# Optimization experiments

Hardware: AMD Instinct MI355X
Metric: run time of the kernel (lower is better)

Reference implementation:

```python
import jax, jax.numpy as jnp
import numpy as np

EMBED_DIM = 4
SEQ_LEN = 14 * 14


def setup_inputs() -> dict:
    key = jax.random.key(0)
    ks = jax.random.split(key, 7)
    B = 32768
    x = jax.random.normal(ks[0], (B, 1, 28, 28), dtype=jnp.float32)
    conv_w = jax.random.normal(ks[1], (4, 1, 2, 2), dtype=jnp.float32) * 0.5
    conv_b = jax.random.normal(ks[2], (4,), dtype=jnp.float32) * 0.1
    rotation_params = jax.random.uniform(ks[3], (16,), dtype=jnp.float32)
    entangle_params = jax.random.uniform(ks[4], (16,), dtype=jnp.float32)
    lin_w = jax.random.normal(ks[5], (10, 784), dtype=jnp.float32) * 0.05
    lin_b = jax.random.normal(ks[6], (10,), dtype=jnp.float32) * 0.05
    return {"x": x, "conv_w": conv_w, "conv_b": conv_b,
            "rotation_params": rotation_params, "entangle_params": entangle_params,
            "lin_w": lin_w, "lin_b": lin_b}


def reference(x, conv_w, conv_b, rotation_params, entangle_params, lin_w, lin_b):
    B = x.shape[0]
    # Quanvolution filter: Conv2d(1,4,k=2,s=2) -> [B,4,14,14]
    feat = jax.lax.conv_general_dilated(
        x, conv_w, window_strides=(2, 2), padding='VALID',
        dimension_numbers=('NCHW', 'OIHW', 'NCHW'))
    feat = feat + conv_b[None, :, None, None]
    # flatten (channel-major like torch .view) then reshape to [B, 196, 4]
    feat = feat.reshape(B, -1).reshape(B, SEQ_LEN, EMBED_DIM)
    # mean embedding per sample: [B, 4]
    mean_embeds = feat.mean(axis=1)
    # classical self-attention on a length-1 sequence per sample
    R = rotation_params.reshape(EMBED_DIM, EMBED_DIM)
    E = entangle_params.reshape(EMBED_DIM, EMBED_DIM)
    q = mean_embeds @ R                               # [B, 4]
    k = mean_embeds @ E                               # [B, 4]
    scores = jnp.einsum('bd,bd->b', q, k) / jnp.sqrt(jnp.float32(EMBED_DIM))
    # softmax over a single-element axis (seq_len == 1) -> all ones, kept for fidelity
    scores = jax.nn.softmax(scores[:, None], axis=-1)  # [B, 1]
    attn_weights = scores * mean_embeds                # [B, 4] (== mean_embeds)
    # broadcast-scale features and classify
    feat = (feat * attn_weights[:, None, :]).reshape(B, -1)  # [B, 784]
    logits = feat @ lin_w.T + lin_b
    return jax.nn.log_softmax(logits, axis=-1)
```

## Files before the change

### kernel.cpp

```cpp
#include <hip/hip_runtime.h>


typedef __attribute__((ext_vector_type(8))) short bf16x8;
typedef __attribute__((ext_vector_type(4))) float f32x4;
typedef __attribute__((ext_vector_type(4))) unsigned int uint4v;

union BU { uint4v u; bf16x8 b; };

__device__ __forceinline__ unsigned short f2bf(float f) {
  unsigned u = __float_as_uint(f);
  unsigned r = u + 0x7FFFu + ((u >> 16) & 1u);
  return (unsigned short)(r >> 16);
}
__device__ __forceinline__ float bf2f(unsigned short h) {
  return __uint_as_float((unsigned)h << 16);
}

#define CST_F 38400
#define A_F   38440

__global__ void qsac_prep(const float* __restrict__ cw, const float* __restrict__ cb,
                          const float* __restrict__ lw, float* __restrict__ wsf) {
  unsigned short* gt = (unsigned short*)wsf;
  const int i = blockIdx.x * 256 + threadIdx.x;
  const int e = i & 7, ln = (i >> 3) & 63, c = i >> 9;
  const int t = c / 3, nt = c - t * 3;
  const int col = nt * 16 + (ln & 15);
  const int k = t * 32 + (ln >> 4) * 8 + e;
  float val = 0.f;
  if (k < 784) {
    const int r = k / 28, cc = k - r * 28;
    const int kh = r & 1, kw = cc & 1;
    const int p = (r >> 1) * 14 + (cc >> 1);
    const int dpix = (2 * ((r >> 1) & 1) + (cc >> 1)) & 3;
    const int cd = col / 12, cj = col - cd * 12;
    if (cd == dpix) {
      const float w0 = cw[(kh << 1) + kw],     w1 = cw[4 + (kh << 1) + kw],
                  w2 = cw[8 + (kh << 1) + kw], w3 = cw[12 + (kh << 1) + kw];
      if (cj < 10)
        val = w0 * lw[cj * 784 + p]       + w1 * lw[cj * 784 + 196 + p] +
              w2 * lw[cj * 784 + 392 + p] + w3 * lw[cj * 784 + 588 + p];
      else if (cj == 10)
        val = (w0 + w1 + w2 + w3) * (1.0f / 196.0f);
    }
  }
  const unsigned short hh = f2bf(val);
  gt[c * 1024 + ln * 8 + e] = hh;
  gt[c * 1024 + 512 + ln * 8 + e] = f2bf(val - bf2f(hh));

  if (blockIdx.x == 0) {
    const int u = threadIdx.x;
    if (u < 40) {
      const int d = u / 10, j = u - (u / 10) * 10;
      const float b0 = cb[0], b1 = cb[1], b2 = cb[2], b3 = cb[3];
      float s = 0.f;
#pragma unroll 7
      for (int q = d; q < 196; q += 4)
        s += b0 * lw[j * 784 + q]       + b1 * lw[j * 784 + 196 + q] +
             b2 * lw[j * 784 + 392 + q] + b3 * lw[j * 784 + 588 + q];
      wsf[CST_F + u] = s;
    } else if (u == 40) {
      wsf[A_F] = (cb[0] + cb[1] + cb[2] + cb[3]) * 0.25f;
    }
  }
}

__global__ __launch_bounds__(1024)
__attribute__((amdgpu_waves_per_eu(4, 4))) void qsac_main(
    const float* __restrict__ x, const float* __restrict__ wsf,
    const float* __restrict__ lin_b, float* __restrict__ out) {
  __shared__ unsigned int smemu[38400];

  const int tid = threadIdx.x;
  const int lane = tid & 63;
  const int wid = __builtin_amdgcn_readfirstlane(tid >> 6);
  const int strip = wid & 7;
  const int khalf = wid >> 3;
  const int nn = lane & 15, kb = lane >> 4;
  const int sbase = blockIdx.x * 128 + strip * 16;
  const float* xrow = x + (size_t)(sbase + nn) * 784;

  {
    const char* wsb = (const char*)wsf;
#pragma unroll
    for (int i = 0; i < 9; ++i) {
      const int cbase = i * 1024 + wid * 64;
      __builtin_amdgcn_global_load_lds(
          (const __attribute__((address_space(1))) unsigned int*)
              (wsb + (size_t)(cbase + lane) * 16),
          (__attribute__((address_space(3))) unsigned int*)&smemu[cbase * 4],
          16, 0, 0);
    }
    if (wid < 6) {
      const int cbase = 9216 + wid * 64;
      __builtin_amdgcn_global_load_lds(
          (const __attribute__((address_space(1))) unsigned int*)
              (wsb + (size_t)(cbase + lane) * 16),
          (__attribute__((address_space(3))) unsigned int*)&smemu[cbase * 4],
          16, 0, 0);
    }
  }
  __syncthreads();

  f32x4 acc[3];
#pragma unroll
  for (int nt = 0; nt < 3; ++nt) acc[nt] = (f32x4){0.f, 0.f, 0.f, 0.f};

  auto tile = [&](const float4& a, const float4& b2, int t) {
    BU bh[3], bl[3];
    const unsigned int* bb = smemu + t * 1536 + lane * 4;
#pragma unroll
    for (int nt = 0; nt < 3; ++nt) {
      bh[nt].u = *(const uint4v*)(bb + nt * 512);
      bl[nt].u = *(const uint4v*)(bb + nt * 512 + 256);
    }
    const float v[8] = {a.x, a.y, a.z, a.w, b2.x, b2.y, b2.z, b2.w};
    bf16x8 Ah, Al;
#pragma unroll
    for (int e = 0; e < 8; ++e) {
      const unsigned short hh = f2bf(v[e]);
      Ah[e] = (short)hh;
      Al[e] = (short)f2bf(v[e] - bf2f(hh));
    }
#pragma unroll
    for (int nt = 0; nt < 3; ++nt) {
      acc[nt] = __builtin_amdgcn_mfma_f32_16x16x32_bf16(Ah, bh[nt].b, acc[nt], 0, 0, 0);
      acc[nt] = __builtin_amdgcn_mfma_f32_16x16x32_bf16(Al, bh[nt].b, acc[nt], 0, 0, 0);
      acc[nt] = __builtin_amdgcn_mfma_f32_16x16x32_bf16(Ah, bl[nt].b, acc[nt], 0, 0, 0);
    }
  };

  auto ldA = [&](int t, float4& a, float4& b2) {
    const int ka = t * 32 + kb * 8;
    const int kc = (ka < 784) ? ka : 0;
    a = *(const float4*)(xrow + kc);
    b2 = *(const float4*)(xrow + kc + 4);
  };

  const int t0 = khalf ? 12 : 0;
  const int t1 = khalf ? 25 : 12;
  float4 xa, xb, na, nb;
  ldA(t0, xa, xb);
#pragma unroll 1
  for (int t = t0; t < t1 - 1; ++t) {
    ldA(t + 1, na, nb);
    tile(xa, xb, t);
    xa = na; xb = nb;
  }
  tile(xa, xb, t1 - 1);

  __syncthreads();
  float* red = (float*)smemu;
  if (khalf == 1) {
#pragma unroll
    for (int nt = 0; nt < 3; ++nt)
#pragma unroll
      for (int rg = 0; rg < 4; ++rg)
        red[(strip * 64 + lane) * 12 + nt * 4 + rg] = acc[nt][rg];
  }
  __syncthreads();
  if (khalf == 0) {
#pragma unroll
    for (int nt = 0; nt < 3; ++nt)
#pragma unroll
      for (int rg = 0; rg < 4; ++rg)
        acc[nt][rg] += red[(strip * 64 + lane) * 12 + nt * 4 + rg];

    float* cx = (float*)smemu + 8192 + strip * (16 * 52);
#pragma unroll
    for (int nt = 0; nt < 3; ++nt)
#pragma unroll
      for (int rg = 0; rg < 4; ++rg)
        cx[(kb * 4 + rg) * 52 + nt * 16 + nn] = acc[nt][rg];
    __builtin_amdgcn_wave_barrier();

    if (lane < 16) {
      float Y[48];
#pragma unroll
      for (int q = 0; q < 12; ++q) {
        const float4 t4 = *(const float4*)&cx[lane * 52 + q * 4];
        Y[q * 4 + 0] = t4.x; Y[q * 4 + 1] = t4.y;
        Y[q * 4 + 2] = t4.z; Y[q * 4 + 3] = t4.w;
      }
      const float a = wsf[A_F];
      float M[4];
#pragma unroll
      for (int d = 0; d < 4; ++d) M[d] = a + Y[d * 12 + 10];
      float logits[10];
#pragma unroll
      for (int j = 0; j < 10; ++j) {
        float vv = lin_b[j];
#pragma unroll
        for (int d = 0; d < 4; ++d)
          vv += M[d] * (wsf[CST_F + d * 10 + j] + Y[d * 12 + j]);
        logits[j] = vv;
      }
      float mx = logits[0];
#pragma unroll
      for (int j = 1; j < 10; ++j) mx = fmaxf(mx, logits[j]);
      float se = 0.f;
#pragma unroll
      for (int j = 0; j < 10; ++j) se += __expf(logits[j] - mx);
      const float lse = mx + __logf(se);
      float* op = out + (size_t)(sbase + lane) * 10;
#pragma unroll
      for (int j = 0; j < 10; ++j) op[j] = logits[j] - lse;
    }
  }
}

extern "C" void kernel_launch(void* const* d_in, const int* in_sizes, int n_in,
                              void* d_out, int out_size, void* d_ws, size_t ws_size,
                              hipStream_t stream) {
  (void)n_in; (void)ws_size; (void)out_size;
  const float* x = (const float*)d_in[0];
  const float* conv_w = (const float*)d_in[1];
  const float* conv_b = (const float*)d_in[2];
  const float* lin_w = (const float*)d_in[5];
  const float* lin_b = (const float*)d_in[6];
  float* out = (float*)d_out;
  float* wsf = (float*)d_ws;

  hipLaunchKernelGGL(qsac_prep, dim3(150), dim3(256), 0, stream,
                     conv_w, conv_b, lin_w, wsf);

  const int B = in_sizes[0] / 784;
  const int nblk = B / 128;
  hipLaunchKernelGGL(qsac_main, dim3(nblk), dim3(1024), 0, stream,
                     x, wsf, lin_b, out);
}
```

Before: 30.35 us.

## Drop split-bf16 error compensation and halve block size to 512 threads

```diff
diff --git a/kernel.cpp b/kernel.cpp
--- a/kernel.cpp
+++ b/kernel.cpp
@@ -6,18 +6,15 @@
 typedef __attribute__((ext_vector_type(4))) unsigned int uint4v;
 
 union BU { uint4v u; bf16x8 b; };
-
-__device__ __forceinline__ unsigned short f2bf(float f) {
-  unsigned u = __float_as_uint(f);
-  unsigned r = u + 0x7FFFu + ((u >> 16) & 1u);
-  return (unsigned short)(r >> 16);
-}
-__device__ __forceinline__ float bf2f(unsigned short h) {
-  return __uint_as_float((unsigned)h << 16);
-}
-
-#define CST_F 38400
-#define A_F   38440
+union AB { unsigned int u[4]; bf16x8 b; };
+
+__device__ __forceinline__ unsigned rne16(float f) {
+  const unsigned u = __float_as_uint(f);
+  return (u + 0x7FFFu + ((u >> 16) & 1u)) >> 16;
+}
+
+#define CST_F 19200
+#define A_F   19240
 
 __global__ void qsac_prep(const float* __restrict__ cw, const float* __restrict__ cb,
                           const float* __restrict__ lw, float* __restrict__ wsf) {
@@ -44,9 +41,7 @@
         val = (w0 + w1 + w2 + w3) * (1.0f / 196.0f);
     }
   }
-  const unsigned short hh = f2bf(val);
-  gt[c * 1024 + ln * 8 + e] = hh;
-  gt[c * 1024 + 512 + ln * 8 + e] = f2bf(val - bf2f(hh));
+  gt[c * 512 + ln * 8 + e] = (unsigned short)rne16(val);
 
   if (blockIdx.x == 0) {
     const int u = threadIdx.x;
@@ -65,39 +60,33 @@
   }
 }
 
-__global__ __launch_bounds__(1024)
+__global__ __launch_bounds__(512)
 __attribute__((amdgpu_waves_per_eu(4, 4))) void qsac_main(
     const float* __restrict__ x, const float* __restrict__ wsf,
     const float* __restrict__ lin_b, float* __restrict__ out) {
-  __shared__ unsigned int smemu[38400];
+  __shared__ unsigned int smemu[19200];
 
   const int tid = threadIdx.x;
   const int lane = tid & 63;
   const int wid = __builtin_amdgcn_readfirstlane(tid >> 6);
-  const int strip = wid & 7;
-  const int khalf = wid >> 3;
+  const int strip = wid & 3;
+  const int khalf = wid >> 2;
   const int nn = lane & 15, kb = lane >> 4;
-  const int sbase = blockIdx.x * 128 + strip * 16;
+  const int sbase = blockIdx.x * 64 + strip * 16;
   const float* xrow = x + (size_t)(sbase + nn) * 784;
 
   {
     const char* wsb = (const char*)wsf;
 #pragma unroll
-    for (int i = 0; i < 9; ++i) {
-      const int cbase = i * 1024 + wid * 64;
-      __builtin_amdgcn_global_load_lds(
-          (const __attribute__((address_space(1))) unsigned int*)
-              (wsb + (size_t)(cbase + lane) * 16),
-          (__attribute__((address_space(3))) unsigned int*)&smemu[cbase * 4],
-          16, 0, 0);
-    }
-    if (wid < 6) {
-      const int cbase = 9216 + wid * 64;
-      __builtin_amdgcn_global_load_lds(
-          (const __attribute__((address_space(1))) unsigned int*)
-              (wsb + (size_t)(cbase + lane) * 16),
-          (__attribute__((address_space(3))) unsigned int*)&smemu[cbase * 4],
-          16, 0, 0);
+    for (int i = 0; i < 10; ++i) {
+      const int c = i * 8 + wid;
+      if (c < 75) {
+        __builtin_amdgcn_global_load_lds(
+            (const __attribute__((address_space(1))) unsigned int*)
+                (wsb + (size_t)(c * 64 + lane) * 16),
+            (__attribute__((address_space(3))) unsigned int*)&smemu[c * 256],
+            16, 0, 0);
+      }
     }
   }
   __syncthreads();
@@ -107,27 +96,18 @@
   for (int nt = 0; nt < 3; ++nt) acc[nt] = (f32x4){0.f, 0.f, 0.f, 0.f};
 
   auto tile = [&](const float4& a, const float4& b2, int t) {
-    BU bh[3], bl[3];
-    const unsigned int* bb = smemu + t * 1536 + lane * 4;
-#pragma unroll
-    for (int nt = 0; nt < 3; ++nt) {
-      bh[nt].u = *(const uint4v*)(bb + nt * 512);
-      bl[nt].u = *(const uint4v*)(bb + nt * 512 + 256);
-    }
-    const float v[8] = {a.x, a.y, a.z, a.w, b2.x, b2.y, b2.z, b2.w};
-    bf16x8 Ah, Al;
-#pragma unroll
-    for (int e = 0; e < 8; ++e) {
-      const unsigned short hh = f2bf(v[e]);
-      Ah[e] = (short)hh;
-      Al[e] = (short)f2bf(v[e] - bf2f(hh));
-    }
-#pragma unroll
-    for (int nt = 0; nt < 3; ++nt) {
-      acc[nt] = __builtin_amdgcn_mfma_f32_16x16x32_bf16(Ah, bh[nt].b, acc[nt], 0, 0, 0);
-      acc[nt] = __builtin_amdgcn_mfma_f32_16x16x32_bf16(Al, bh[nt].b, acc[nt], 0, 0, 0);
-      acc[nt] = __builtin_amdgcn_mfma_f32_16x16x32_bf16(Ah, bl[nt].b, acc[nt], 0, 0, 0);
-    }
+    BU bh[3];
+    const unsigned int* bb = smemu + t * 768 + lane * 4;
+#pragma unroll
+    for (int nt = 0; nt < 3; ++nt) bh[nt].u = *(const uint4v*)(bb + nt * 256);
+    AB Ah;
+    Ah.u[0] = rne16(a.x)  | (rne16(a.y)  << 16);
+    Ah.u[1] = rne16(a.z)  | (rne16(a.w)  << 16);
+    Ah.u[2] = rne16(b2.x) | (rne16(b2.y) << 16);
+    Ah.u[3] = rne16(b2.z) | (rne16(b2.w) << 16);
+#pragma unroll
+    for (int nt = 0; nt < 3; ++nt)
+      acc[nt] = __builtin_amdgcn_mfma_f32_16x16x32_bf16(Ah.b, bh[nt].b, acc[nt], 0, 0, 0);
   };
 
   auto ldA = [&](int t, float4& a, float4& b2) {
@@ -166,7 +146,7 @@
       for (int rg = 0; rg < 4; ++rg)
         acc[nt][rg] += red[(strip * 64 + lane) * 12 + nt * 4 + rg];
 
-    float* cx = (float*)smemu + 8192 + strip * (16 * 52);
+    float* cx = (float*)smemu + 3072 + strip * (16 * 52);
 #pragma unroll
     for (int nt = 0; nt < 3; ++nt)
 #pragma unroll
@@ -225,7 +205,7 @@
                      conv_w, conv_b, lin_w, wsf);
 
   const int B = in_sizes[0] / 784;
-  const int nblk = B / 128;
-  hipLaunchKernelGGL(qsac_main, dim3(nblk), dim3(1024), 0, stream,
+  const int nblk = B / 64;
+  hipLaunchKernelGGL(qsac_main, dim3(nblk), dim3(512), 0, stream,
                      x, wsf, lin_b, out);
 }
```

Measured after the change: 29.46 us. 2.9% less time.
